# Optimization experiments

Hardware: AMD Instinct MI355X
Metric: run time of the kernel (lower is better)

The kernel has to match this reference:

```python
import jax, jax.numpy as jnp
import numpy as np

B, L, D, A = 4, 4096, 256, 64  # batch, seq_len, n_embd, att_size

def setup_inputs() -> dict:
    key = jax.random.key(0)
    kx, kq, kk, kv = jax.random.split(key, 4)
    x = jax.random.normal(kx, (B, L, D), dtype=jnp.float32)
    # torch nn.Linear(n_embd, att_size) weight is [att_size, n_embd]; we store transposed [D, A]
    s = 1.0 / np.sqrt(D)
    Wq = jax.random.normal(kq, (D, A), dtype=jnp.float32) * s
    Wk = jax.random.normal(kk, (D, A), dtype=jnp.float32) * s
    Wv = jax.random.normal(kv, (D, A), dtype=jnp.float32) * s
    return {"x": x, "Wq": Wq, "Wk": Wk, "Wv": Wv}

def reference(x, Wq, Wk, Wv):
    # q,k,v: [B,L,A]
    q = jnp.einsum('bld,da->bla', x, Wq)
    k = jnp.einsum('bld,da->bla', x, Wk)
    v = jnp.einsum('bld,da->bla', x, Wv)
    # NOTE: original module does NOT scale by 1/sqrt(att_size)
    scores = jnp.einsum('bqa,bka->bqk', q, k)  # [B,L,L]
    Lq = x.shape[1]
    causal = jnp.tril(jnp.ones((Lq, Lq), dtype=bool))
    scores = jnp.where(causal, scores, -jnp.inf)
    weights = jax.nn.softmax(scores, axis=-1)
    # dropout is identity in eval mode
    out = jnp.einsum('bqk,bka->bqa', weights, v)  # [B,L,A]
    return out
```

## Files before the change

### kernel.cpp

```cpp
#include <hip/hip_runtime.h>
#include <math.h>

#define B_ 4
#define L_ 4096
#define D_ 256
#define A_ 64
#define M_ (B_*L_)

typedef _Float16 half4 __attribute__((ext_vector_type(4)));
typedef _Float16 half8 __attribute__((ext_vector_type(8)));
typedef __attribute__((ext_vector_type(4))) float floatx4;

__device__ __forceinline__ unsigned short f2h_(float f) {
    _Float16 h = (_Float16)f;
    return __builtin_bit_cast(unsigned short, h);
}

__global__ __launch_bounds__(256) void wconv_kernel(
    const float* __restrict__ Wq, const float* __restrict__ Wk,
    const float* __restrict__ Wv, unsigned short* __restrict__ wt)
{
    const int w = blockIdx.x, t = threadIdx.x;
    const float* W = (w == 0) ? Wq : (w == 1) ? Wk : Wv;
    unsigned short* o = wt + w * A_ * D_;
    const float scale = (w == 0) ? 1.44269504f : 1.0f;
    __shared__ float T[A_ * 260];
    #pragma unroll
    for (int p = 0; p < 16; ++p) {
        int idx = p * 256 + t;
        int d = idx >> 4, a4 = (idx & 15) * 4;
        float4 v = *(const float4*)(W + d * A_ + a4);
        T[(a4 + 0) * 260 + d] = v.x * scale;
        T[(a4 + 1) * 260 + d] = v.y * scale;
        T[(a4 + 2) * 260 + d] = v.z * scale;
        T[(a4 + 3) * 260 + d] = v.w * scale;
    }
    __syncthreads();
    const int a = t >> 2, d0 = (t & 3) * 64;
    #pragma unroll
    for (int i = 0; i < 16; ++i) {
        float4 v = *(const float4*)(&T[a * 260 + d0 + 4 * i]);
        ushort4 s;
        s.x = f2h_(v.x); s.y = f2h_(v.y); s.z = f2h_(v.z); s.w = f2h_(v.w);
        *(ushort4*)(o + a * D_ + d0 + 4 * i) = s;
    }
}

__global__ __launch_bounds__(256) void proj_kernel(
    const float* __restrict__ x,
    const unsigned short* __restrict__ wt,
    unsigned short* __restrict__ qo,
    unsigned short* __restrict__ ko,
    unsigned short* __restrict__ vto)
{
    __shared__ __align__(16) unsigned short sh[2 * 64 * 264];
    unsigned short* Xh = sh;
    unsigned short* Ws = sh + 64 * 264;
    const int t = threadIdx.x, m0 = blockIdx.x * 64, w = blockIdx.y;

    #pragma unroll
    for (int p = 0; p < 16; ++p) {
        int idx = p * 1024 + t * 4;
        int row = idx >> 8, col = idx & 255;
        float4 v = *(const float4*)(x + (size_t)(m0 + row) * D_ + col);
        ushort4 s;
        s.x = f2h_(v.x); s.y = f2h_(v.y); s.z = f2h_(v.z); s.w = f2h_(v.w);
        *(ushort4*)(Xh + row * 264 + col) = s;
    }
    const unsigned short* wsrc = wt + w * A_ * D_;
    #pragma unroll
    for (int i = 0; i < 8; ++i) {
        int idx = i * 256 + t;
        int row = idx >> 5, col = (idx & 31) * 8;
        *(uint4*)(Ws + row * 264 + col) = *(const uint4*)(wsrc + row * D_ + col);
    }
    __syncthreads();

    const int lane = t & 63, wid = t >> 6, c = lane & 15, g = lane >> 4;
    half8 xa[8];
    #pragma unroll
    for (int s = 0; s < 8; ++s)
        xa[s] = *(const half8*)(Xh + (16 * wid + c) * 264 + 32 * s + 8 * g);

    #pragma unroll
    for (int nt = 0; nt < 4; ++nt) {
        floatx4 acc = {0.f, 0.f, 0.f, 0.f};
        #pragma unroll
        for (int s = 0; s < 8; ++s) {
            half8 wb = *(const half8*)(Ws + (16 * nt + c) * 264 + 32 * s + 8 * g);
            acc = __builtin_amdgcn_mfma_f32_16x16x32_f16(xa[s], wb, acc, 0, 0, 0);
        }
        if (w < 2) {
            unsigned short* o = (w == 0) ? qo : ko;
            #pragma unroll
            for (int r = 0; r < 4; ++r)
                o[(size_t)(m0 + 16 * wid + 4 * g + r) * A_ + 16 * nt + c] = f2h_(acc[r]);
        } else {
            const int bb = m0 >> 12, l0 = m0 & (L_ - 1);
            #pragma unroll
            for (int r = 0; r < 4; ++r)
                vto[((size_t)(bb * A_ + 16 * nt + c)) * L_ + l0 + 16 * wid + 4 * g + r] = f2h_(acc[r]);
        }
    }
}

__global__ __launch_bounds__(256) void attn_kernel(
    const unsigned short* __restrict__ qb,
    const unsigned short* __restrict__ kb,
    const unsigned short* __restrict__ vt,
    float* __restrict__ out)
{
    __shared__ __align__(16) unsigned short smem[4 * 4608];
    unsigned short* Ks = smem;
    unsigned short* Vs = smem + 2 * 4608;

    const int t    = threadIdx.x;
    const int lane = t & 63;
    const int wid  = t >> 6;
    const int qsub = wid >> 1;
    const int ph   = wid & 1;
    const int c    = lane & 15;
    const int g    = lane >> 4;
    const int b    = blockIdx.y;
    const int qt   = (gridDim.x - 1) - blockIdx.x;
    const int q0   = qt * 32;
    const int qrow0 = q0 + qsub * 16;
    const int qme  = qrow0 + c;

    const size_t base  = (size_t)b * L_ * A_;
    const size_t vbase = (size_t)b * A_ * L_;

    half8 qf[2];
    {
        const unsigned short* qp = qb + base + (size_t)(qrow0 + c) * A_ + g * 8;
        qf[0] = *(const half8*)(qp);
        qf[1] = *(const half8*)(qp + 32);
    }

    floatx4 O4[4];
    #pragma unroll
    for (int at = 0; at < 4; ++at) O4[at] = (floatx4){0.f, 0.f, 0.f, 0.f};
    float m_ = -INFINITY, l_ = 0.f;

    const int Tmax  = ((q0 + 31) >> 6) + 1;
    const int nIt   = (Tmax + 1) >> 1;
    const int ktmax = (qrow0 + 15) >> 6;

    for (int it = 0; it < nIt; ++it) {
        __syncthreads();
        #pragma unroll
        for (int tile = 0; tile < 2; ++tile) {
            const int kts = 2 * it + tile;
            if (kts < Tmax) {
                const int k0s = kts << 6;
                #pragma unroll
                for (int i = 0; i < 2; ++i) {
                    const int cid = t + (i << 8);
                    const int row = cid >> 3, c8 = cid & 7;
                    uint4 d = *(const uint4*)(kb + base + (size_t)k0s * 64 + cid * 8);
                    *(uint4*)(Ks + tile * 4608 + row * 72 + c8 * 8) = d;
                }
                #pragma unroll
                for (int i = 0; i < 2; ++i) {
                    const int cid = t + (i << 8);
                    const int row = cid >> 3, c8 = cid & 7;
                    uint4 d = *(const uint4*)(vt + vbase + (size_t)row * L_ + k0s + c8 * 8);
                    const int nt = c8 >> 1, g0 = 2 * (c8 & 1);
                    const int col0 = 16 * g0 + 4 * nt;
                    uint2 lo; lo.x = d.x; lo.y = d.y;
                    uint2 hi; hi.x = d.z; hi.y = d.w;
                    *(uint2*)(Vs + tile * 4608 + row * 72 + col0)      = lo;
                    *(uint2*)(Vs + tile * 4608 + row * 72 + col0 + 16) = hi;
                }
            }
        }
        __syncthreads();

        const int kt = 2 * it + ph;
        if (kt > ktmax) continue;
        const int k0 = kt << 6;
        const unsigned short* Kw = Ks + ph * 4608;
        const unsigned short* Vw = Vs + ph * 4608;

        floatx4 S4[4];
        #pragma unroll
        for (int nt = 0; nt < 4; ++nt) S4[nt] = (floatx4){0.f, 0.f, 0.f, 0.f};
        #pragma unroll
        for (int s = 0; s < 2; ++s) {
            #pragma unroll
            for (int nt = 0; nt < 4; ++nt) {
                half8 kf = *(const half8*)(Kw + (16 * nt + c) * 72 + 32 * s + 8 * g);
                S4[nt] = __builtin_amdgcn_mfma_f32_16x16x32_f16(kf, qf[s], S4[nt], 0, 0, 0);
            }
        }

        if (k0 + 63 > qrow0) {
            #pragma unroll
            for (int nt = 0; nt < 4; ++nt)
                #pragma unroll
                for (int r = 0; r < 4; ++r)
                    if (k0 + 16 * nt + 4 * g + r > qme) S4[nt][r] = -INFINITY;
        }

        float tm = fmaxf(fmaxf(fmaxf(S4[0][0], S4[0][1]), fmaxf(S4[0][2], S4[0][3])),
                         fmaxf(fmaxf(S4[1][0], S4[1][1]), fmaxf(S4[1][2], S4[1][3])));
        tm = fmaxf(tm, fmaxf(fmaxf(fmaxf(S4[2][0], S4[2][1]), fmaxf(S4[2][2], S4[2][3])),
                             fmaxf(fmaxf(S4[3][0], S4[3][1]), fmaxf(S4[3][2], S4[3][3]))));
        tm = fmaxf(tm, __shfl_xor(tm, 16));
        tm = fmaxf(tm, __shfl_xor(tm, 32));
        const float mn  = fmaxf(m_, tm);
        const float mnc = fmaxf(mn, -3.0e38f);
        const float al  = exp2f(fminf(m_ - mnc, 0.f));
        float rs = 0.f;
        half4 pf[4];
        #pragma unroll
        for (int nt = 0; nt < 4; ++nt) {
            #pragma unroll
            for (int r = 0; r < 4; ++r) {
                float p = exp2f(S4[nt][r] - mnc);
                S4[nt][r] = p;
                rs += p;
            }
            pf[nt][0] = (_Float16)S4[nt][0];
            pf[nt][1] = (_Float16)S4[nt][1];
            pf[nt][2] = (_Float16)S4[nt][2];
            pf[nt][3] = (_Float16)S4[nt][3];
        }
        rs += __shfl_xor(rs, 16);
        rs += __shfl_xor(rs, 32);
        l_ = l_ * al + rs;
        m_ = mn;
        #pragma unroll
        for (int at = 0; at < 4; ++at) O4[at] *= al;

        #pragma unroll
        for (int at = 0; at < 4; ++at) {
            half8 v01 = *(const half8*)(Vw + (16 * at + c) * 72 + 16 * g);
            half8 v23 = *(const half8*)(Vw + (16 * at + c) * 72 + 16 * g + 8);
            half4 va0 = __builtin_shufflevector(v01, v01, 0, 1, 2, 3);
            half4 va1 = __builtin_shufflevector(v01, v01, 4, 5, 6, 7);
            half4 va2 = __builtin_shufflevector(v23, v23, 0, 1, 2, 3);
            half4 va3 = __builtin_shufflevector(v23, v23, 4, 5, 6, 7);
            O4[at] = __builtin_amdgcn_mfma_f32_16x16x16f16(va0, pf[0], O4[at], 0, 0, 0);
            O4[at] = __builtin_amdgcn_mfma_f32_16x16x16f16(va1, pf[1], O4[at], 0, 0, 0);
            O4[at] = __builtin_amdgcn_mfma_f32_16x16x16f16(va2, pf[2], O4[at], 0, 0, 0);
            O4[at] = __builtin_amdgcn_mfma_f32_16x16x16f16(va3, pf[3], O4[at], 0, 0, 0);
        }
    }

    __syncthreads();
    float4* Obuf = (float4*)smem;
    float2* mlb  = (float2*)(smem + 4096);
    float*  Ot   = (float*)(smem + 4608);

    if (ph == 1) {
        #pragma unroll
        for (int at = 0; at < 4; ++at) {
            float4 v; v.x = O4[at][0]; v.y = O4[at][1]; v.z = O4[at][2]; v.w = O4[at][3];
            Obuf[at * 128 + qsub * 64 + lane] = v;
        }
        float2 ml; ml.x = m_; ml.y = l_;
        mlb[qsub * 64 + lane] = ml;
    }
    __syncthreads();
    if (ph == 0) {
        const float2 ml1 = mlb[qsub * 64 + lane];
        const float mf = fmaxf(m_, ml1.x);
        const float a0 = (m_ == mf)    ? 1.f : exp2f(m_ - mf);
        const float a1 = (ml1.x == mf) ? 1.f : exp2f(ml1.x - mf);
        const float inv = 1.f / (l_ * a0 + ml1.y * a1);
        #pragma unroll
        for (int at = 0; at < 4; ++at) {
            const float4 o1 = Obuf[at * 128 + qsub * 64 + lane];
            const float o1r[4] = {o1.x, o1.y, o1.z, o1.w};
            #pragma unroll
            for (int r = 0; r < 4; ++r)
                Ot[(qsub * 16 + c) * 68 + 16 * at + 4 * g + r] =
                    (O4[at][r] * a0 + o1r[r] * a1) * inv;
        }
    }
    __syncthreads();
    {
        const int qr = t >> 3, ccol = (t & 7) * 8;
        float4 u0 = *(const float4*)(Ot + qr * 68 + ccol);
        float4 u1 = *(const float4*)(Ot + qr * 68 + ccol + 4);
        float* op = out + base + (size_t)(q0 + qr) * A_ + ccol;
        *(float4*)(op)     = u0;
        *(float4*)(op + 4) = u1;
    }
}

extern "C" void kernel_launch(void* const* d_in, const int* in_sizes, int n_in,
                              void* d_out, int out_size, void* d_ws, size_t ws_size,
                              hipStream_t stream) {
    const float* x  = (const float*)d_in[0];
    const float* Wq = (const float*)d_in[1];
    const float* Wk = (const float*)d_in[2];
    const float* Wv = (const float*)d_in[3];

    unsigned short* qb = (unsigned short*)d_ws;
    unsigned short* kb = qb + (size_t)M_ * A_;
    unsigned short* vt = kb + (size_t)M_ * A_;
    unsigned short* wt = vt + (size_t)M_ * A_;
    float* out = (float*)d_out;

    hipLaunchKernelGGL(wconv_kernel, dim3(3), dim3(256), 0, stream, Wq, Wk, Wv, wt);

    dim3 gp(M_ / 64, 3), bp(256);
    hipLaunchKernelGGL(proj_kernel, gp, bp, 0, stream, x, wt, qb, kb, vt);

    dim3 ga(L_ / 32, B_), ba(256);
    hipLaunchKernelGGL(attn_kernel, ga, ba, 0, stream, qb, kb, vt, out);
}
```

Baseline: 142.8 us.

## Split KV range across four waves per 16-query tile, load K/V directly to registers

The attention kernel now handles 16 query rows per block, with each of the four waves processing every fourth 64-key tile and loading K and V fragments straight from global memory instead of staging them through shared memory with block-wide barriers. Partial softmax states from the four waves are merged in shared memory at the end. The projection kernel reads weights directly from global memory and stages its output through shared memory so that global stores are coalesced 16-byte writes. The aim is to remove per-iteration synchronisation and improve causal load balance, at the cost of redundant global/L2 traffic for K/V and a heavier final merge.

```diff
diff --git a/kernel.cpp b/kernel.cpp
--- a/kernel.cpp
+++ b/kernel.cpp
@@ -53,9 +53,8 @@
     unsigned short* __restrict__ ko,
     unsigned short* __restrict__ vto)
 {
-    __shared__ __align__(16) unsigned short sh[2 * 64 * 264];
-    unsigned short* Xh = sh;
-    unsigned short* Ws = sh + 64 * 264;
+    __shared__ __align__(16) unsigned short Xh[64 * 264];
+    __shared__ __align__(16) unsigned short Cst[64 * 72];
     const int t = threadIdx.x, m0 = blockIdx.x * 64, w = blockIdx.y;
 
     #pragma unroll
@@ -67,13 +66,6 @@
         s.x = f2h_(v.x); s.y = f2h_(v.y); s.z = f2h_(v.z); s.w = f2h_(v.w);
         *(ushort4*)(Xh + row * 264 + col) = s;
     }
-    const unsigned short* wsrc = wt + w * A_ * D_;
-    #pragma unroll
-    for (int i = 0; i < 8; ++i) {
-        int idx = i * 256 + t;
-        int row = idx >> 5, col = (idx & 31) * 8;
-        *(uint4*)(Ws + row * 264 + col) = *(const uint4*)(wsrc + row * D_ + col);
-    }
     __syncthreads();
 
     const int lane = t & 63, wid = t >> 6, c = lane & 15, g = lane >> 4;
@@ -82,25 +74,40 @@
     for (int s = 0; s < 8; ++s)
         xa[s] = *(const half8*)(Xh + (16 * wid + c) * 264 + 32 * s + 8 * g);
 
+    const unsigned short* wsrc = wt + w * A_ * D_;
     #pragma unroll
     for (int nt = 0; nt < 4; ++nt) {
         floatx4 acc = {0.f, 0.f, 0.f, 0.f};
         #pragma unroll
         for (int s = 0; s < 8; ++s) {
-            half8 wb = *(const half8*)(Ws + (16 * nt + c) * 264 + 32 * s + 8 * g);
+            half8 wb = *(const half8*)(wsrc + (16 * nt + c) * D_ + 32 * s + 8 * g);
             acc = __builtin_amdgcn_mfma_f32_16x16x32_f16(xa[s], wb, acc, 0, 0, 0);
         }
         if (w < 2) {
-            unsigned short* o = (w == 0) ? qo : ko;
             #pragma unroll
             for (int r = 0; r < 4; ++r)
-                o[(size_t)(m0 + 16 * wid + 4 * g + r) * A_ + 16 * nt + c] = f2h_(acc[r]);
+                Cst[(16 * wid + 4 * g + r) * 72 + 16 * nt + c] = f2h_(acc[r]);
         } else {
-            const int bb = m0 >> 12, l0 = m0 & (L_ - 1);
             #pragma unroll
             for (int r = 0; r < 4; ++r)
-                vto[((size_t)(bb * A_ + 16 * nt + c)) * L_ + l0 + 16 * wid + 4 * g + r] = f2h_(acc[r]);
-        }
+                Cst[(16 * nt + c) * 72 + 16 * wid + 4 * g + r] = f2h_(acc[r]);
+        }
+    }
+    __syncthreads();
+
+    const int row = t >> 2, seg = t & 3;
+    uint4 d0 = *(const uint4*)(Cst + row * 72 + seg * 16);
+    uint4 d1 = *(const uint4*)(Cst + row * 72 + seg * 16 + 8);
+    if (w < 2) {
+        unsigned short* o = (w == 0) ? qo : ko;
+        unsigned short* p = o + (size_t)(m0 + row) * A_ + seg * 16;
+        *(uint4*)(p) = d0;
+        *(uint4*)(p + 8) = d1;
+    } else {
+        const int bb = m0 >> 12, l0 = m0 & (L_ - 1);
+        unsigned short* p = vto + ((size_t)(bb * A_ + row)) * L_ + l0 + seg * 16;
+        *(uint4*)(p) = d0;
+        *(uint4*)(p + 8) = d1;
     }
 }
 
@@ -110,29 +117,26 @@
     const unsigned short* __restrict__ vt,
     float* __restrict__ out)
 {
-    __shared__ __align__(16) unsigned short smem[4 * 4608];
-    unsigned short* Ks = smem;
-    unsigned short* Vs = smem + 2 * 4608;
+    __shared__ __align__(16) float4 Obuf[4][4][64];
+    __shared__ float2 mlb[4][64];
+    __shared__ float  Ot[16 * 68];
 
     const int t    = threadIdx.x;
     const int lane = t & 63;
     const int wid  = t >> 6;
-    const int qsub = wid >> 1;
-    const int ph   = wid & 1;
     const int c    = lane & 15;
     const int g    = lane >> 4;
     const int b    = blockIdx.y;
     const int qt   = (gridDim.x - 1) - blockIdx.x;
-    const int q0   = qt * 32;
-    const int qrow0 = q0 + qsub * 16;
-    const int qme  = qrow0 + c;
+    const int q0   = qt * 16;
+    const int qme  = q0 + c;
 
     const size_t base  = (size_t)b * L_ * A_;
     const size_t vbase = (size_t)b * A_ * L_;
 
     half8 qf[2];
     {
-        const unsigned short* qp = qb + base + (size_t)(qrow0 + c) * A_ + g * 8;
+        const unsigned short* qp = qb + base + (size_t)(q0 + c) * A_ + g * 8;
         qf[0] = *(const half8*)(qp);
         qf[1] = *(const half8*)(qp + 32);
     }
@@ -142,59 +146,37 @@
     for (int at = 0; at < 4; ++at) O4[at] = (floatx4){0.f, 0.f, 0.f, 0.f};
     float m_ = -INFINITY, l_ = 0.f;
 
-    const int Tmax  = ((q0 + 31) >> 6) + 1;
-    const int nIt   = (Tmax + 1) >> 1;
-    const int ktmax = (qrow0 + 15) >> 6;
-
-    for (int it = 0; it < nIt; ++it) {
-        __syncthreads();
-        #pragma unroll
-        for (int tile = 0; tile < 2; ++tile) {
-            const int kts = 2 * it + tile;
-            if (kts < Tmax) {
-                const int k0s = kts << 6;
-                #pragma unroll
-                for (int i = 0; i < 2; ++i) {
-                    const int cid = t + (i << 8);
-                    const int row = cid >> 3, c8 = cid & 7;
-                    uint4 d = *(const uint4*)(kb + base + (size_t)k0s * 64 + cid * 8);
-                    *(uint4*)(Ks + tile * 4608 + row * 72 + c8 * 8) = d;
-                }
-                #pragma unroll
-                for (int i = 0; i < 2; ++i) {
-                    const int cid = t + (i << 8);
-                    const int row = cid >> 3, c8 = cid & 7;
-                    uint4 d = *(const uint4*)(vt + vbase + (size_t)row * L_ + k0s + c8 * 8);
-                    const int nt = c8 >> 1, g0 = 2 * (c8 & 1);
-                    const int col0 = 16 * g0 + 4 * nt;
-                    uint2 lo; lo.x = d.x; lo.y = d.y;
-                    uint2 hi; hi.x = d.z; hi.y = d.w;
-                    *(uint2*)(Vs + tile * 4608 + row * 72 + col0)      = lo;
-                    *(uint2*)(Vs + tile * 4608 + row * 72 + col0 + 16) = hi;
-                }
-            }
-        }
-        __syncthreads();
-
-        const int kt = 2 * it + ph;
-        if (kt > ktmax) continue;
+    const int T = (q0 >> 6) + 1;
+
+    for (int kt = wid; kt < T; kt += 4) {
         const int k0 = kt << 6;
-        const unsigned short* Kw = Ks + ph * 4608;
-        const unsigned short* Vw = Vs + ph * 4608;
+        const unsigned short* kp = kb + base + (size_t)k0 * A_;
+        const unsigned short* vp = vt + vbase + k0;
+
+        half8 kf[2][4];
+        #pragma unroll
+        for (int s = 0; s < 2; ++s)
+            #pragma unroll
+            for (int nt = 0; nt < 4; ++nt)
+                kf[s][nt] = *(const half8*)(kp + (16 * nt + c) * A_ + 32 * s + 8 * g);
 
         floatx4 S4[4];
         #pragma unroll
         for (int nt = 0; nt < 4; ++nt) S4[nt] = (floatx4){0.f, 0.f, 0.f, 0.f};
         #pragma unroll
-        for (int s = 0; s < 2; ++s) {
-            #pragma unroll
-            for (int nt = 0; nt < 4; ++nt) {
-                half8 kf = *(const half8*)(Kw + (16 * nt + c) * 72 + 32 * s + 8 * g);
-                S4[nt] = __builtin_amdgcn_mfma_f32_16x16x32_f16(kf, qf[s], S4[nt], 0, 0, 0);
-            }
-        }
-
-        if (k0 + 63 > qrow0) {
+        for (int s = 0; s < 2; ++s)
+            #pragma unroll
+            for (int nt = 0; nt < 4; ++nt)
+                S4[nt] = __builtin_amdgcn_mfma_f32_16x16x32_f16(kf[s][nt], qf[s], S4[nt], 0, 0, 0);
+
+        half4 vf[4][4];
+        #pragma unroll
+        for (int at = 0; at < 4; ++at)
+            #pragma unroll
+            for (int nt = 0; nt < 4; ++nt)
+                vf[at][nt] = *(const half4*)(vp + (size_t)(16 * at + c) * L_ + 16 * nt + 4 * g);
+
+        if (kt == T - 1) {
             #pragma unroll
             for (int nt = 0; nt < 4; ++nt)
                 #pragma unroll
@@ -230,63 +212,51 @@
         rs += __shfl_xor(rs, 32);
         l_ = l_ * al + rs;
         m_ = mn;
-        #pragma unroll
-        for (int at = 0; at < 4; ++at) O4[at] *= al;
 
         #pragma unroll
         for (int at = 0; at < 4; ++at) {
-            half8 v01 = *(const half8*)(Vw + (16 * at + c) * 72 + 16 * g);
-            half8 v23 = *(const half8*)(Vw + (16 * at + c) * 72 + 16 * g + 8);
-            half4 va0 = __builtin_shufflevector(v01, v01, 0, 1, 2, 3);
-            half4 va1 = __builtin_shufflevector(v01, v01, 4, 5, 6, 7);
-            half4 va2 = __builtin_shufflevector(v23, v23, 0, 1, 2, 3);
-            half4 va3 = __builtin_shufflevector(v23, v23, 4, 5, 6, 7);
-            O4[at] = __builtin_amdgcn_mfma_f32_16x16x16f16(va0, pf[0], O4[at], 0, 0, 0);
-            O4[at] = __builtin_amdgcn_mfma_f32_16x16x16f16(va1, pf[1], O4[at], 0, 0, 0);
-            O4[at] = __builtin_amdgcn_mfma_f32_16x16x16f16(va2, pf[2], O4[at], 0, 0, 0);
-            O4[at] = __builtin_amdgcn_mfma_f32_16x16x16f16(va3, pf[3], O4[at], 0, 0, 0);
-        }
-    }
-
-    __syncthreads();
-    float4* Obuf = (float4*)smem;
-    float2* mlb  = (float2*)(smem + 4096);
-    float*  Ot   = (float*)(smem + 4608);
-
-    if (ph == 1) {
-        #pragma unroll
-        for (int at = 0; at < 4; ++at) {
-            float4 v; v.x = O4[at][0]; v.y = O4[at][1]; v.z = O4[at][2]; v.w = O4[at][3];
-            Obuf[at * 128 + qsub * 64 + lane] = v;
-        }
-        float2 ml; ml.x = m_; ml.y = l_;
-        mlb[qsub * 64 + lane] = ml;
-    }
-    __syncthreads();
-    if (ph == 0) {
-        const float2 ml1 = mlb[qsub * 64 + lane];
-        const float mf = fmaxf(m_, ml1.x);
-        const float a0 = (m_ == mf)    ? 1.f : exp2f(m_ - mf);
-        const float a1 = (ml1.x == mf) ? 1.f : exp2f(ml1.x - mf);
-        const float inv = 1.f / (l_ * a0 + ml1.y * a1);
-        #pragma unroll
-        for (int at = 0; at < 4; ++at) {
-            const float4 o1 = Obuf[at * 128 + qsub * 64 + lane];
-            const float o1r[4] = {o1.x, o1.y, o1.z, o1.w};
-            #pragma unroll
-            for (int r = 0; r < 4; ++r)
-                Ot[(qsub * 16 + c) * 68 + 16 * at + 4 * g + r] =
-                    (O4[at][r] * a0 + o1r[r] * a1) * inv;
-        }
-    }
-    __syncthreads();
+            O4[at] *= al;
+            O4[at] = __builtin_amdgcn_mfma_f32_16x16x16f16(vf[at][0], pf[0], O4[at], 0, 0, 0);
+            O4[at] = __builtin_amdgcn_mfma_f32_16x16x16f16(vf[at][1], pf[1], O4[at], 0, 0, 0);
+            O4[at] = __builtin_amdgcn_mfma_f32_16x16x16f16(vf[at][2], pf[2], O4[at], 0, 0, 0);
+            O4[at] = __builtin_amdgcn_mfma_f32_16x16x16f16(vf[at][3], pf[3], O4[at], 0, 0, 0);
+        }
+    }
+
+    #pragma unroll
+    for (int at = 0; at < 4; ++at) {
+        float4 v; v.x = O4[at][0]; v.y = O4[at][1]; v.z = O4[at][2]; v.w = O4[at][3];
+        Obuf[wid][at][lane] = v;
+    }
+    float2 ml; ml.x = m_; ml.y = l_;
+    mlb[wid][lane] = ml;
+    __syncthreads();
+
     {
-        const int qr = t >> 3, ccol = (t & 7) * 8;
-        float4 u0 = *(const float4*)(Ot + qr * 68 + ccol);
-        float4 u1 = *(const float4*)(Ot + qr * 68 + ccol + 4);
-        float* op = out + base + (size_t)(q0 + qr) * A_ + ccol;
-        *(float4*)(op)     = u0;
-        *(float4*)(op + 4) = u1;
+        const int at = t >> 6, ls = t & 63;
+        const int lc = ls & 15, lg = ls >> 4;
+        float mf = fmaxf(fmaxf(mlb[0][ls].x, mlb[1][ls].x),
+                         fmaxf(mlb[2][ls].x, mlb[3][ls].x));
+        float lf = 0.f;
+        float acc[4] = {0.f, 0.f, 0.f, 0.f};
+        #pragma unroll
+        for (int ph = 0; ph < 4; ++ph) {
+            const float wgt = exp2f(mlb[ph][ls].x - mf);
+            lf += wgt * mlb[ph][ls].y;
+            const float4 o = Obuf[ph][at][ls];
+            acc[0] += wgt * o.x; acc[1] += wgt * o.y;
+            acc[2] += wgt * o.z; acc[3] += wgt * o.w;
+        }
+        const float inv = 1.f / lf;
+        #pragma unroll
+        for (int r = 0; r < 4; ++r)
+            Ot[lc * 68 + 16 * at + 4 * lg + r] = acc[r] * inv;
+    }
+    __syncthreads();
+    {
+        const int q = t >> 4, col = (t & 15) * 4;
+        float4 u = *(const float4*)(Ot + q * 68 + col);
+        *(float4*)(out + base + (size_t)(q0 + q) * A_ + col) = u;
     }
 }
 
@@ -309,6 +279,6 @@
     dim3 gp(M_ / 64, 3), bp(256);
     hipLaunchKernelGGL(proj_kernel, gp, bp, 0, stream, x, wt, qb, kb, vt);
 
-    dim3 ga(L_ / 32, B_), ba(256);
+    dim3 ga(L_ / 16, B_), ba(256);
     hipLaunchKernelGGL(attn_kernel, ga, ba, 0, stream, qb, kb, vt, out);
 }
```

Result: slower. 212.8 us (+49.0%).

## Split causal KV range across two blocks and merge partial softmax results

Applied to the files above, without the earlier changes.

The attention grid doubles so each query tile's key range is divided between two blocks. Each block writes unnormalized partial outputs plus max/sum statistics, and a new merge kernel combines them. This is meant to balance the causal workload and raise occupancy. The projection kernel now reads x once per 32-row block for all three weights via 6 warps, reads weights directly from global, and stages outputs in LDS for coalesced stores. The V tile load drops its shuffled LDS layout. In exchange there is an extra kernel launch and extra global traffic for the partial outputs.

```diff
diff --git a/kernel.cpp b/kernel.cpp
--- a/kernel.cpp
+++ b/kernel.cpp
@@ -46,61 +46,75 @@
     }
 }
 
-__global__ __launch_bounds__(256) void proj_kernel(
+__global__ __launch_bounds__(384) void proj_kernel(
     const float* __restrict__ x,
     const unsigned short* __restrict__ wt,
     unsigned short* __restrict__ qo,
     unsigned short* __restrict__ ko,
     unsigned short* __restrict__ vto)
 {
-    __shared__ __align__(16) unsigned short sh[2 * 64 * 264];
-    unsigned short* Xh = sh;
-    unsigned short* Ws = sh + 64 * 264;
-    const int t = threadIdx.x, m0 = blockIdx.x * 64, w = blockIdx.y;
-
-    #pragma unroll
-    for (int p = 0; p < 16; ++p) {
-        int idx = p * 1024 + t * 4;
-        int row = idx >> 8, col = idx & 255;
-        float4 v = *(const float4*)(x + (size_t)(m0 + row) * D_ + col);
-        ushort4 s;
-        s.x = f2h_(v.x); s.y = f2h_(v.y); s.z = f2h_(v.z); s.w = f2h_(v.w);
-        *(ushort4*)(Xh + row * 264 + col) = s;
-    }
+    __shared__ __align__(16) unsigned short Xh[32 * 264];
+    __shared__ __align__(16) unsigned short Cst[6 * 1536];
+    const int t = threadIdx.x, m0 = blockIdx.x * 32;
+
+    #pragma unroll
+    for (int p = 0; p < 6; ++p) {
+        int idx = p * 384 + t;
+        if (idx < 2048) {
+            int row = idx >> 6, col = (idx & 63) * 4;
+            float4 v = *(const float4*)(x + (size_t)(m0 + row) * D_ + col);
+            ushort4 s;
+            s.x = f2h_(v.x); s.y = f2h_(v.y); s.z = f2h_(v.z); s.w = f2h_(v.w);
+            *(ushort4*)(Xh + row * 264 + col) = s;
+        }
+    }
+    __syncthreads();
+
+    const int wid = t >> 6, lane = t & 63, c = lane & 15, g = lane >> 4;
+    const int w = wid >> 1, mt = wid & 1;
+
+    half8 xa[8];
+    #pragma unroll
+    for (int s = 0; s < 8; ++s)
+        xa[s] = *(const half8*)(Xh + (16 * mt + c) * 264 + 32 * s + 8 * g);
+
     const unsigned short* wsrc = wt + w * A_ * D_;
-    #pragma unroll
-    for (int i = 0; i < 8; ++i) {
-        int idx = i * 256 + t;
-        int row = idx >> 5, col = (idx & 31) * 8;
-        *(uint4*)(Ws + row * 264 + col) = *(const uint4*)(wsrc + row * D_ + col);
-    }
-    __syncthreads();
-
-    const int lane = t & 63, wid = t >> 6, c = lane & 15, g = lane >> 4;
-    half8 xa[8];
-    #pragma unroll
-    for (int s = 0; s < 8; ++s)
-        xa[s] = *(const half8*)(Xh + (16 * wid + c) * 264 + 32 * s + 8 * g);
-
+    unsigned short* Cw = Cst + wid * 1536;
     #pragma unroll
     for (int nt = 0; nt < 4; ++nt) {
         floatx4 acc = {0.f, 0.f, 0.f, 0.f};
         #pragma unroll
         for (int s = 0; s < 8; ++s) {
-            half8 wb = *(const half8*)(Ws + (16 * nt + c) * 264 + 32 * s + 8 * g);
+            half8 wb = *(const half8*)(wsrc + (16 * nt + c) * D_ + 32 * s + 8 * g);
             acc = __builtin_amdgcn_mfma_f32_16x16x32_f16(xa[s], wb, acc, 0, 0, 0);
         }
         if (w < 2) {
-            unsigned short* o = (w == 0) ? qo : ko;
             #pragma unroll
             for (int r = 0; r < 4; ++r)
-                o[(size_t)(m0 + 16 * wid + 4 * g + r) * A_ + 16 * nt + c] = f2h_(acc[r]);
+                Cw[(4 * g + r) * 72 + 16 * nt + c] = f2h_(acc[r]);
         } else {
-            const int bb = m0 >> 12, l0 = m0 & (L_ - 1);
             #pragma unroll
             for (int r = 0; r < 4; ++r)
-                vto[((size_t)(bb * A_ + 16 * nt + c)) * L_ + l0 + 16 * wid + 4 * g + r] = f2h_(acc[r]);
-        }
+                Cw[(16 * nt + c) * 24 + 4 * g + r] = f2h_(acc[r]);
+        }
+    }
+
+    if (w < 2) {
+        unsigned short* o = (w == 0) ? qo : ko;
+        const int row16 = lane >> 2, seg = lane & 3;
+        uint4 d0 = *(const uint4*)(Cw + row16 * 72 + seg * 16);
+        uint4 d1 = *(const uint4*)(Cw + row16 * 72 + seg * 16 + 8);
+        unsigned short* p = o + (size_t)(m0 + 16 * mt + row16) * A_ + seg * 16;
+        *(uint4*)(p) = d0;
+        *(uint4*)(p + 8) = d1;
+    }
+    __syncthreads();
+    if (t < 256) {
+        const int a = t >> 2, quarter = t & 3;
+        const int o = quarter * 8, mtv = o >> 4, idx = o & 15;
+        uint4 d = *(const uint4*)(Cst + (4 + mtv) * 1536 + a * 24 + idx);
+        const int bb = m0 >> 12, l0 = m0 & (L_ - 1);
+        *(uint4*)(vto + ((size_t)(bb * A_ + a)) * L_ + l0 + o) = d;
     }
 }
 
@@ -108,7 +122,10 @@
     const unsigned short* __restrict__ qb,
     const unsigned short* __restrict__ kb,
     const unsigned short* __restrict__ vt,
-    float* __restrict__ out)
+    float* __restrict__ out,
+    float* __restrict__ po1,
+    float2* __restrict__ ml0,
+    float2* __restrict__ ml1)
 {
     __shared__ __align__(16) unsigned short smem[4 * 4608];
     unsigned short* Ks = smem;
@@ -122,9 +139,11 @@
     const int c    = lane & 15;
     const int g    = lane >> 4;
     const int b    = blockIdx.y;
-    const int qt   = (gridDim.x - 1) - blockIdx.x;
+    const int bx   = blockIdx.x;
+    const int qt   = 127 - (bx >> 1);
+    const int h    = bx & 1;
     const int q0   = qt * 32;
-    const int qrow0 = q0 + qsub * 16;
+    const int qrow0 = q0 + 16 * qsub;
     const int qme  = qrow0 + c;
 
     const size_t base  = (size_t)b * L_ * A_;
@@ -142,42 +161,35 @@
     for (int at = 0; at < 4; ++at) O4[at] = (floatx4){0.f, 0.f, 0.f, 0.f};
     float m_ = -INFINITY, l_ = 0.f;
 
-    const int Tmax  = ((q0 + 31) >> 6) + 1;
-    const int nIt   = (Tmax + 1) >> 1;
-    const int ktmax = (qrow0 + 15) >> 6;
+    const int T   = (q0 >> 6) + 1;
+    const int Th  = (T + 1) >> 1;
+    const int t0  = h ? Th : 0;
+    const int t1  = h ? T : Th;
+    const int nIt = (t1 - t0 + 1) >> 1;
+    const int Tm1 = T - 1;
 
     for (int it = 0; it < nIt; ++it) {
         __syncthreads();
         #pragma unroll
         for (int tile = 0; tile < 2; ++tile) {
-            const int kts = 2 * it + tile;
-            if (kts < Tmax) {
+            const int kts = t0 + 2 * it + tile;
+            if (kts < t1) {
                 const int k0s = kts << 6;
                 #pragma unroll
                 for (int i = 0; i < 2; ++i) {
                     const int cid = t + (i << 8);
                     const int row = cid >> 3, c8 = cid & 7;
-                    uint4 d = *(const uint4*)(kb + base + (size_t)k0s * 64 + cid * 8);
-                    *(uint4*)(Ks + tile * 4608 + row * 72 + c8 * 8) = d;
-                }
-                #pragma unroll
-                for (int i = 0; i < 2; ++i) {
-                    const int cid = t + (i << 8);
-                    const int row = cid >> 3, c8 = cid & 7;
-                    uint4 d = *(const uint4*)(vt + vbase + (size_t)row * L_ + k0s + c8 * 8);
-                    const int nt = c8 >> 1, g0 = 2 * (c8 & 1);
-                    const int col0 = 16 * g0 + 4 * nt;
-                    uint2 lo; lo.x = d.x; lo.y = d.y;
-                    uint2 hi; hi.x = d.z; hi.y = d.w;
-                    *(uint2*)(Vs + tile * 4608 + row * 72 + col0)      = lo;
-                    *(uint2*)(Vs + tile * 4608 + row * 72 + col0 + 16) = hi;
+                    uint4 dK = *(const uint4*)(kb + base + (size_t)k0s * 64 + cid * 8);
+                    *(uint4*)(Ks + tile * 4608 + row * 72 + c8 * 8) = dK;
+                    uint4 dV = *(const uint4*)(vt + vbase + (size_t)row * L_ + k0s + c8 * 8);
+                    *(uint4*)(Vs + tile * 4608 + row * 72 + c8 * 8) = dV;
                 }
             }
         }
         __syncthreads();
 
-        const int kt = 2 * it + ph;
-        if (kt > ktmax) continue;
+        const int kt = t0 + 2 * it + ph;
+        if (kt >= t1) continue;
         const int k0 = kt << 6;
         const unsigned short* Kw = Ks + ph * 4608;
         const unsigned short* Vw = Vs + ph * 4608;
@@ -186,15 +198,14 @@
         #pragma unroll
         for (int nt = 0; nt < 4; ++nt) S4[nt] = (floatx4){0.f, 0.f, 0.f, 0.f};
         #pragma unroll
-        for (int s = 0; s < 2; ++s) {
+        for (int s = 0; s < 2; ++s)
             #pragma unroll
             for (int nt = 0; nt < 4; ++nt) {
                 half8 kf = *(const half8*)(Kw + (16 * nt + c) * 72 + 32 * s + 8 * g);
                 S4[nt] = __builtin_amdgcn_mfma_f32_16x16x32_f16(kf, qf[s], S4[nt], 0, 0, 0);
             }
-        }
-
-        if (k0 + 63 > qrow0) {
+
+        if (kt == Tm1) {
             #pragma unroll
             for (int nt = 0; nt < 4; ++nt)
                 #pragma unroll
@@ -230,64 +241,79 @@
         rs += __shfl_xor(rs, 32);
         l_ = l_ * al + rs;
         m_ = mn;
-        #pragma unroll
-        for (int at = 0; at < 4; ++at) O4[at] *= al;
 
         #pragma unroll
         for (int at = 0; at < 4; ++at) {
-            half8 v01 = *(const half8*)(Vw + (16 * at + c) * 72 + 16 * g);
-            half8 v23 = *(const half8*)(Vw + (16 * at + c) * 72 + 16 * g + 8);
-            half4 va0 = __builtin_shufflevector(v01, v01, 0, 1, 2, 3);
-            half4 va1 = __builtin_shufflevector(v01, v01, 4, 5, 6, 7);
-            half4 va2 = __builtin_shufflevector(v23, v23, 0, 1, 2, 3);
-            half4 va3 = __builtin_shufflevector(v23, v23, 4, 5, 6, 7);
-            O4[at] = __builtin_amdgcn_mfma_f32_16x16x16f16(va0, pf[0], O4[at], 0, 0, 0);
-            O4[at] = __builtin_amdgcn_mfma_f32_16x16x16f16(va1, pf[1], O4[at], 0, 0, 0);
-            O4[at] = __builtin_amdgcn_mfma_f32_16x16x16f16(va2, pf[2], O4[at], 0, 0, 0);
-            O4[at] = __builtin_amdgcn_mfma_f32_16x16x16f16(va3, pf[3], O4[at], 0, 0, 0);
-        }
-    }
-
-    __syncthreads();
-    float4* Obuf = (float4*)smem;
-    float2* mlb  = (float2*)(smem + 4096);
-    float*  Ot   = (float*)(smem + 4608);
-
-    if (ph == 1) {
-        #pragma unroll
-        for (int at = 0; at < 4; ++at) {
-            float4 v; v.x = O4[at][0]; v.y = O4[at][1]; v.z = O4[at][2]; v.w = O4[at][3];
-            Obuf[at * 128 + qsub * 64 + lane] = v;
-        }
-        float2 ml; ml.x = m_; ml.y = l_;
-        mlb[qsub * 64 + lane] = ml;
-    }
-    __syncthreads();
-    if (ph == 0) {
-        const float2 ml1 = mlb[qsub * 64 + lane];
-        const float mf = fmaxf(m_, ml1.x);
-        const float a0 = (m_ == mf)    ? 1.f : exp2f(m_ - mf);
-        const float a1 = (ml1.x == mf) ? 1.f : exp2f(ml1.x - mf);
-        const float inv = 1.f / (l_ * a0 + ml1.y * a1);
-        #pragma unroll
-        for (int at = 0; at < 4; ++at) {
-            const float4 o1 = Obuf[at * 128 + qsub * 64 + lane];
-            const float o1r[4] = {o1.x, o1.y, o1.z, o1.w};
-            #pragma unroll
-            for (int r = 0; r < 4; ++r)
-                Ot[(qsub * 16 + c) * 68 + 16 * at + 4 * g + r] =
-                    (O4[at][r] * a0 + o1r[r] * a1) * inv;
-        }
-    }
-    __syncthreads();
+            O4[at] *= al;
+            #pragma unroll
+            for (int nt = 0; nt < 4; ++nt) {
+                half4 va = *(const half4*)(Vw + (16 * at + c) * 72 + 16 * nt + 4 * g);
+                O4[at] = __builtin_amdgcn_mfma_f32_16x16x16f16(va, pf[nt], O4[at], 0, 0, 0);
+            }
+        }
+    }
+
+    __syncthreads();
+    float*  Of  = (float*)smem;
+    float2* mlb = (float2*)(smem + 8192);
+    #pragma unroll
+    for (int at = 0; at < 4; ++at) {
+        float4 v; v.x = O4[at][0]; v.y = O4[at][1]; v.z = O4[at][2]; v.w = O4[at][3];
+        ((float4*)Of)[wid * 256 + at * 64 + lane] = v;
+    }
+    if (g == 0) { float2 ml; ml.x = m_; ml.y = l_; mlb[wid * 16 + c] = ml; }
+    __syncthreads();
+
     {
-        const int qr = t >> 3, ccol = (t & 7) * 8;
-        float4 u0 = *(const float4*)(Ot + qr * 68 + ccol);
-        float4 u1 = *(const float4*)(Ot + qr * 68 + ccol + 4);
-        float* op = out + base + (size_t)(q0 + qr) * A_ + ccol;
-        *(float4*)(op)     = u0;
-        *(float4*)(op + 4) = u1;
-    }
+        const int q32 = t >> 3, seg = t & 7;
+        const int qs = q32 >> 4, cc = q32 & 15;
+        const float2 A0 = mlb[(2 * qs) * 16 + cc];
+        const float2 A1 = mlb[(2 * qs + 1) * 16 + cc];
+        const float mf = fmaxf(A0.x, A1.x);
+        const float mc = fmaxf(mf, -3.0e38f);
+        const float w0 = exp2f(A0.x - mc);
+        const float w1 = exp2f(A1.x - mc);
+        const float ls = w0 * A0.y + w1 * A1.y;
+        float res[8];
+        #pragma unroll
+        for (int u = 0; u < 8; ++u) {
+            const int a = seg * 8 + u;
+            const int at = a >> 4, gg = (a >> 2) & 3, r = a & 3;
+            const int i0 = ((2 * qs) * 256 + at * 64 + gg * 16 + cc) * 4 + r;
+            const int i1 = ((2 * qs + 1) * 256 + at * 64 + gg * 16 + cc) * 4 + r;
+            res[u] = w0 * Of[i0] + w1 * Of[i1];
+        }
+        float* PO = h ? po1 : out;
+        float* p = PO + (base + (size_t)(q0 + q32) * A_) + seg * 8;
+        *(float4*)(p)     = make_float4(res[0], res[1], res[2], res[3]);
+        *(float4*)(p + 4) = make_float4(res[4], res[5], res[6], res[7]);
+        if (seg == 0) {
+            float2 ml; ml.x = mf; ml.y = ls;
+            (h ? ml1 : ml0)[b * L_ + q0 + q32] = ml;
+        }
+    }
+}
+
+__global__ __launch_bounds__(256) void merge_kernel(
+    float* __restrict__ out, const float* __restrict__ po1,
+    const float2* __restrict__ ml0, const float2* __restrict__ ml1)
+{
+    const int tg = blockIdx.x * 256 + threadIdx.x;
+    const int q = tg >> 4;
+    const float2 a0 = ml0[q], a1 = ml1[q];
+    const float mf = fmaxf(a0.x, a1.x);
+    const float mc = fmaxf(mf, -3.0e38f);
+    const float w0 = exp2f(a0.x - mc);
+    const float w1 = exp2f(a1.x - mc);
+    const float inv = 1.f / (w0 * a0.y + w1 * a1.y);
+    float4 o0 = ((const float4*)out)[tg];
+    float4 o1 = ((const float4*)po1)[tg];
+    float4 r;
+    r.x = (o0.x * w0 + o1.x * w1) * inv;
+    r.y = (o0.y * w0 + o1.y * w1) * inv;
+    r.z = (o0.z * w0 + o1.z * w1) * inv;
+    r.w = (o0.w * w0 + o1.w * w1) * inv;
+    ((float4*)out)[tg] = r;
 }
 
 extern "C" void kernel_launch(void* const* d_in, const int* in_sizes, int n_in,
@@ -298,17 +324,19 @@
     const float* Wk = (const float*)d_in[2];
     const float* Wv = (const float*)d_in[3];
 
-    unsigned short* qb = (unsigned short*)d_ws;
-    unsigned short* kb = qb + (size_t)M_ * A_;
-    unsigned short* vt = kb + (size_t)M_ * A_;
-    unsigned short* wt = vt + (size_t)M_ * A_;
+    char* ws = (char*)d_ws;
+    unsigned short* qb = (unsigned short*)(ws);
+    unsigned short* kb = (unsigned short*)(ws + (2u << 20));
+    unsigned short* vt = (unsigned short*)(ws + (4u << 20));
+    unsigned short* wt = (unsigned short*)(ws + (6u << 20));
+    float*  po1 = (float*) (ws + (6u << 20) + 98304);
+    float2* ml0 = (float2*)(ws + (6u << 20) + 98304 + (4u << 20));
+    float2* ml1 = (float2*)(ws + (6u << 20) + 98304 + (4u << 20) + 131072);
     float* out = (float*)d_out;
 
     hipLaunchKernelGGL(wconv_kernel, dim3(3), dim3(256), 0, stream, Wq, Wk, Wv, wt);
-
-    dim3 gp(M_ / 64, 3), bp(256);
-    hipLaunchKernelGGL(proj_kernel, gp, bp, 0, stream, x, wt, qb, kb, vt);
-
-    dim3 ga(L_ / 32, B_), ba(256);
-    hipLaunchKernelGGL(attn_kernel, ga, ba, 0, stream, qb, kb, vt, out);
-}
+    hipLaunchKernelGGL(proj_kernel, dim3(M_ / 32), dim3(384), 0, stream, x, wt, qb, kb, vt);
+    hipLaunchKernelGGL(attn_kernel, dim3(256, B_), dim3(256), 0, stream,
+                       qb, kb, vt, out, po1, ml0, ml1);
+    hipLaunchKernelGGL(merge_kernel, dim3(1024), dim3(256), 0, stream, out, po1, ml0, ml1);
+}
```

Result: faster. 138.1 us (-3.3%).
